# Optimization experiments

Measured on AMD Instinct MI355X. Metric: run time of the kernel, lower is better.

The kernel has to match this reference:

```python
import jax, jax.numpy as jnp
import numpy as np


def _binarize_ste(t):
    # torch code overwrites .data with sign(), which acts as a straight-through
    # identity for autograd: forward = sign(t), backward = identity.
    return t + jax.lax.stop_gradient(jnp.sign(t) - t)


def setup_inputs() -> dict:
    key = jax.random.key(0)
    k1, k2 = jax.random.split(key)
    B, C_IN, C_OUT = 512, 1536, 512
    x = jax.random.normal(k1, (B, C_IN), dtype=jnp.float32)
    stdv = 1.0 / np.sqrt(C_OUT * C_IN)
    weight = jax.random.uniform(k2, (C_OUT, C_IN), dtype=jnp.float32,
                                minval=-stdv, maxval=stdv)
    return {"x": x, "weight": weight}


def reference(x, weight):
    B, c_in = x.shape
    c_out = weight.shape[0]
    G = c_in // 3  # majority-3 group count
    bx = _binarize_ste(x)        # [B, c_in] in {-1, 0, +1}
    bw = _binarize_ste(weight)   # [c_out, c_in]
    # einsum('bj,cj->bcj') then group-sum over triples == contract only within
    # each group of 3, never materializing the full [B, c_out, c_in] tensor.
    inter = jnp.einsum('bgk,cgk->bcg',
                       bx.reshape(B, G, 3),
                       bw.reshape(c_out, G, 3))  # [B, c_out, G]
    out = 2.25 * jnp.sum(jnp.clip(inter, -1.0, 1.0), axis=-1)  # [B, c_out]
    return out
```

## Files before the change

### kernel.cpp

```cpp
#include <hip/hip_runtime.h>
#include <hip/hip_bf16.h>
#include <stdint.h>


#define CIN   1536
#define B_DIM 512
#define COUT  512
#define WORDS 64
#define STRIDE 66

__global__ __launch_bounds__(256) void pack_kernel(
    const float* __restrict__ x, const float* __restrict__ w,
    uint2* __restrict__ px, uint2* __restrict__ pw) {
  __shared__ float buf[4 * CIN];
  int bid = blockIdx.x;
  const float* src;
  uint2* dst;
  int row0;
  if (bid < 128) { src = x;  dst = px; row0 = bid * 4; }
  else           { src = w;  dst = pw; row0 = (bid - 128) * 4; }

  const float4* s4 = (const float4*)(src + (size_t)row0 * CIN);
  float4* b4 = (float4*)buf;
  #pragma unroll
  for (int i = threadIdx.x; i < 4 * CIN / 4; i += 256) b4[i] = s4[i];
  __syncthreads();

  int r  = threadIdx.x >> 6;
  int wd = threadIdx.x & 63;
  const float* rowp = buf + r * CIN + wd * 24;
  unsigned P = 0, N = 0;
  #pragma unroll
  for (int k = 0; k < 24; k++) {
    float v = rowp[k];
    unsigned bit = (unsigned)((k / 3) * 4 + (k % 3));
    P |= (v > 0.0f ? 1u : 0u) << bit;
    N |= (v < 0.0f ? 1u : 0u) << bit;
  }
  dst[(size_t)(row0 + r) * WORDS + wd] = make_uint2(P, N);
}

__device__ __forceinline__ void maj3_word(unsigned xp, unsigned xn,
                                          unsigned wp, unsigned wn,
                                          int& acc_gt, int& acc_ge) {
  const unsigned M1 = 0x11111111u, M8 = 0x88888888u;
  unsigned pos = (xp & wp) | (xn & wn);
  unsigned neg = (xp & wn) | (xn & wp);
  unsigned cp = (pos & M1) + ((pos >> 1) & M1) + ((pos >> 2) & M1);
  unsigned cn = (neg & M1) + ((neg >> 1) & M1) + ((neg >> 2) & M1);
  unsigned u = (cp | M8) - cn;
  unsigned t = u - M1;
  acc_gt += __popc(t & M8);
  acc_ge += __popc(u & M8);
}

__global__ __launch_bounds__(256) void maj3_kernel(
    const uint2* __restrict__ px, const uint2* __restrict__ pw,
    float* __restrict__ out) {
  __shared__ __align__(16) uint2 sx[16][STRIDE];
  __shared__ __align__(16) uint2 sw[16][STRIDE];

  const int b0 = blockIdx.y * 16;
  const int c0 = blockIdx.x * 16;
  const int tid = threadIdx.x;

  #pragma unroll
  for (int i = tid; i < 16 * WORDS; i += 256) {
    int r = i >> 6, wd = i & 63;
    sx[r][wd] = px[(size_t)(b0 + r) * WORDS + wd];
    sw[r][wd] = pw[(size_t)(c0 + r) * WORDS + wd];
  }
  __syncthreads();

  const int tx = tid & 15;
  const int ty = tid >> 4;

  int acc_gt = 0, acc_ge = 0;

  const uint4* xrow = (const uint4*)&sx[ty][0];
  const uint4* wrow = (const uint4*)&sw[tx][0];

  #pragma unroll
  for (int i = 0; i < WORDS / 2; i++) {
    uint4 xa = xrow[i];
    uint4 wb = wrow[i];
    maj3_word(xa.x, xa.y, wb.x, wb.y, acc_gt, acc_ge);
    maj3_word(xa.z, xa.w, wb.z, wb.w, acc_gt, acc_ge);
  }

  out[(size_t)(b0 + ty) * COUT + (c0 + tx)] =
      2.25f * (float)(acc_gt + acc_ge - 512);
}

extern "C" void kernel_launch(void* const* d_in, const int* in_sizes, int n_in,
                              void* d_out, int out_size, void* d_ws, size_t ws_size,
                              hipStream_t stream) {
  const float* x = (const float*)d_in[0];
  const float* w = (const float*)d_in[1];
  float* out = (float*)d_out;

  uint2* px = (uint2*)d_ws;
  uint2* pw = px + (size_t)B_DIM * WORDS;

  pack_kernel<<<256, 256, 0, stream>>>(x, w, px, pw);

  dim3 grid(COUT / 16, B_DIM / 16);
  maj3_kernel<<<grid, 256, 0, stream>>>(px, pw, out);
}
```

Before: 72.72 us.

## Pack ten triples per word and compute two output rows per thread

Repacks the binarized signs densely as 10 three-bit groups per 32-bit word, dropping row length from 64 to 52 words, and adjusts the SWAR majority masks and the constant offset to account for padded groups. The compute kernel now tiles 32x16 outputs per block, so each thread reuses its weight row for two batch rows. This cuts the per-output bitwise work and shared-memory traffic, at the cost of a tail word and fewer blocks.

```diff
diff --git a/kernel.cpp b/kernel.cpp
--- a/kernel.cpp
+++ b/kernel.cpp
@@ -3,11 +3,11 @@
 #include <stdint.h>
 
 
-#define CIN   1536
-#define B_DIM 512
-#define COUT  512
-#define WORDS 64
-#define STRIDE 66
+#define CIN    1536
+#define B_DIM  512
+#define COUT   512
+#define WORDS3 52
+#define WSTRIDE 54
 
 __global__ __launch_bounds__(256) void pack_kernel(
     const float* __restrict__ x, const float* __restrict__ w,
@@ -28,68 +28,86 @@
 
   int r  = threadIdx.x >> 6;
   int wd = threadIdx.x & 63;
-  const float* rowp = buf + r * CIN + wd * 24;
-  unsigned P = 0, N = 0;
-  #pragma unroll
-  for (int k = 0; k < 24; k++) {
-    float v = rowp[k];
-    unsigned bit = (unsigned)((k / 3) * 4 + (k % 3));
-    P |= (v > 0.0f ? 1u : 0u) << bit;
-    N |= (v < 0.0f ? 1u : 0u) << bit;
+  if (wd < WORDS3) {
+    const float* rowp = buf + r * CIN + wd * 30;
+    int nmax = CIN - wd * 30;
+    unsigned P = 0, N = 0;
+    #pragma unroll
+    for (int k = 0; k < 30; k++) {
+      if (k < nmax) {
+        float v = rowp[k];
+        P |= (v > 0.0f ? 1u : 0u) << k;
+        N |= (v < 0.0f ? 1u : 0u) << k;
+      }
+    }
+    dst[(size_t)(row0 + r) * WORDS3 + wd] = make_uint2(P, N);
   }
-  dst[(size_t)(row0 + r) * WORDS + wd] = make_uint2(P, N);
 }
 
-__device__ __forceinline__ void maj3_word(unsigned xp, unsigned xn,
-                                          unsigned wp, unsigned wn,
-                                          int& acc_gt, int& acc_ge) {
-  const unsigned M1 = 0x11111111u, M8 = 0x88888888u;
+__device__ __forceinline__ void maj3w(unsigned xp, unsigned xn,
+                                      unsigned wp, unsigned wn,
+                                      int& gt, int& ge) {
+  const unsigned M1 = 0x09249249u;
+  const unsigned M4 = 0x24924924u;
   unsigned pos = (xp & wp) | (xn & wn);
   unsigned neg = (xp & wn) | (xn & wp);
   unsigned cp = (pos & M1) + ((pos >> 1) & M1) + ((pos >> 2) & M1);
   unsigned cn = (neg & M1) + ((neg >> 1) & M1) + ((neg >> 2) & M1);
-  unsigned u = (cp | M8) - cn;
+  unsigned u = (cp | M4) - cn;
   unsigned t = u - M1;
-  acc_gt += __popc(t & M8);
-  acc_ge += __popc(u & M8);
+  gt += __popc(t & M4);
+  ge += __popc(u & M4);
 }
 
 __global__ __launch_bounds__(256) void maj3_kernel(
     const uint2* __restrict__ px, const uint2* __restrict__ pw,
     float* __restrict__ out) {
-  __shared__ __align__(16) uint2 sx[16][STRIDE];
-  __shared__ __align__(16) uint2 sw[16][STRIDE];
+  __shared__ __align__(16) uint2 sx[32][WSTRIDE];
+  __shared__ __align__(16) uint2 sw[16][WSTRIDE];
 
-  const int b0 = blockIdx.y * 16;
+  const int b0 = blockIdx.y * 32;
   const int c0 = blockIdx.x * 16;
   const int tid = threadIdx.x;
 
+  const uint4* gx = (const uint4*)(px + (size_t)b0 * WORDS3);
+  const uint4* gw = (const uint4*)(pw + (size_t)c0 * WORDS3);
+  uint4* lx = (uint4*)sx;
+  uint4* lw = (uint4*)sw;
   #pragma unroll
-  for (int i = tid; i < 16 * WORDS; i += 256) {
-    int r = i >> 6, wd = i & 63;
-    sx[r][wd] = px[(size_t)(b0 + r) * WORDS + wd];
-    sw[r][wd] = pw[(size_t)(c0 + r) * WORDS + wd];
+  for (int i = tid; i < 32 * 26; i += 256) {
+    int r = i / 26, wd = i - r * 26;
+    lx[r * 27 + wd] = gx[i];
+  }
+  #pragma unroll
+  for (int i = tid; i < 16 * 26; i += 256) {
+    int r = i / 26, wd = i - r * 26;
+    lw[r * 27 + wd] = gw[i];
   }
   __syncthreads();
 
   const int tx = tid & 15;
   const int ty = tid >> 4;
 
-  int acc_gt = 0, acc_ge = 0;
-
-  const uint4* xrow = (const uint4*)&sx[ty][0];
-  const uint4* wrow = (const uint4*)&sw[tx][0];
+  int gt0 = 0, ge0 = 0, gt1 = 0, ge1 = 0;
+  const uint4* x0 = (const uint4*)&sx[ty][0];
+  const uint4* x1 = (const uint4*)&sx[ty + 16][0];
+  const uint4* wr = (const uint4*)&sw[tx][0];
 
   #pragma unroll
-  for (int i = 0; i < WORDS / 2; i++) {
-    uint4 xa = xrow[i];
-    uint4 wb = wrow[i];
-    maj3_word(xa.x, xa.y, wb.x, wb.y, acc_gt, acc_ge);
-    maj3_word(xa.z, xa.w, wb.z, wb.w, acc_gt, acc_ge);
+  for (int i = 0; i < 26; i++) {
+    uint4 a0 = x0[i];
+    uint4 a1 = x1[i];
+    uint4 b  = wr[i];
+    maj3w(a0.x, a0.y, b.x, b.y, gt0, ge0);
+    maj3w(a0.z, a0.w, b.z, b.w, gt0, ge0);
+    maj3w(a1.x, a1.y, b.x, b.y, gt1, ge1);
+    maj3w(a1.z, a1.w, b.z, b.w, gt1, ge1);
   }
 
   out[(size_t)(b0 + ty) * COUT + (c0 + tx)] =
-      2.25f * (float)(acc_gt + acc_ge - 512);
+      2.25f * (float)(gt0 + ge0 - 520);
+  out[(size_t)(b0 + ty + 16) * COUT + (c0 + tx)] =
+      2.25f * (float)(gt1 + ge1 - 520);
 }
 
 extern "C" void kernel_launch(void* const* d_in, const int* in_sizes, int n_in,
@@ -100,10 +118,10 @@
   float* out = (float*)d_out;
 
   uint2* px = (uint2*)d_ws;
-  uint2* pw = px + (size_t)B_DIM * WORDS;
+  uint2* pw = px + (size_t)B_DIM * WORDS3;
 
   pack_kernel<<<256, 256, 0, stream>>>(x, w, px, pw);
 
-  dim3 grid(COUT / 16, B_DIM / 16);
+  dim3 grid(COUT / 16, B_DIM / 32);
   maj3_kernel<<<grid, 256, 0, stream>>>(px, pw, out);
 }
```

Measured after the change: 71.60 us. Within noise of the previous version (-1.5%).
